# Optimization experiments

Hardware: AMD Instinct MI355X
Metric: run time of the kernel (lower is better)

The kernel has to match this reference:

```python
import jax, jax.numpy as jnp
import numpy as np

IS_CAUSAL = True
NEG_INF = float('-inf')


def setup_inputs() -> dict:
    key = jax.random.key(0)
    kq, kk, kv = jax.random.split(key, 3)
    B, H, S, D = 4, 16, 2048, 64
    return {
        'query': jax.random.normal(kq, (B, H, S, D), dtype=jnp.float32),
        'key': jax.random.normal(kk, (B, H, S, D), dtype=jnp.float32),
        'value': jax.random.normal(kv, (B, H, S, D), dtype=jnp.float32),
    }


def reference(query, key, value):
    # Attention(Q,K,V) = softmax(QK^T / sqrt(d_k) + causal_mask) V
    d_k = query.shape[-1]
    scale = 1.0 / np.sqrt(d_k).astype(np.float32)
    # [B,H,Sq,Sk]
    scores = jnp.einsum('bhqd,bhkd->bhqk', query, key) * scale
    if IS_CAUSAL:
        sq, sk = query.shape[-2], key.shape[-2]
        causal = jnp.triu(jnp.ones((sq, sk), dtype=bool), k=1)
        scores = jnp.where(causal[None, None, :, :], NEG_INF, scores)
    weights = jax.nn.softmax(scores, axis=-1)
    # dropout p=0.0 (eval): identity
    out = jnp.einsum('bhqk,bhkd->bhqd', weights, value)
    return out
```

## Files before the change

### kernel.cpp

```cpp
#include <hip/hip_runtime.h>
#include <stdint.h>


#define SLEN 2048
#define DHEAD 64
#define NHEADS 64
#define NELEM (SLEN * DHEAD * NHEADS)
#define PADP 72

typedef short bf16x8 __attribute__((ext_vector_type(8)));
typedef float f32x4 __attribute__((ext_vector_type(4)));

__device__ __forceinline__ uint32_t pkbf(float hi, float lo) {
    uint32_t a = __builtin_bit_cast(uint32_t, lo) + 0x8000u;
    uint32_t b = __builtin_bit_cast(uint32_t, hi) + 0x8000u;
    return __builtin_amdgcn_perm(b, a, 0x07060302u);
}
__device__ __forceinline__ unsigned short f2bf(float f) {
    return (unsigned short)((__builtin_bit_cast(uint32_t, f) + 0x8000u) >> 16);
}
__device__ __forceinline__ int swz(int row, int g) {
    return row * 64 + ((g ^ (row & 7)) << 3);
}

__global__ __launch_bounds__(256)
void convert_prep(const float* __restrict__ K, const float* __restrict__ V,
                  unsigned short* __restrict__ Kb, unsigned short* __restrict__ Vtb) {
    __shared__ unsigned short Lt[64 * 264];
    const int b = blockIdx.x, t = threadIdx.x;
    if (b < 4096) {
        const int off = (b * 256 + t) * 8;
        float4 a = *(const float4*)(K + off);
        float4 c = *(const float4*)(K + off + 4);
        uint4 o;
        o.x = pkbf(a.y, a.x); o.y = pkbf(a.w, a.z);
        o.z = pkbf(c.y, c.x); o.w = pkbf(c.w, c.z);
        *(uint4*)(Kb + off) = o;
    } else {
        const int vb2 = b - 4096;
        const int head = vb2 >> 3, kblk = vb2 & 7;
        const float* Vh = V + (size_t)head * (SLEN * DHEAD) + kblk * 256 * DHEAD;
        unsigned short* Vo = Vtb + (size_t)head * (SLEN * DHEAD) + kblk * 256;
#pragma unroll
        for (int i = 0; i < 16; ++i) {
            int idx = t + 256 * i;
            int key = idx >> 4, d4 = idx & 15;
            float4 v = *(const float4*)(Vh + key * DHEAD + d4 * 4);
            Lt[(d4 * 4 + 0) * 264 + key] = f2bf(v.x);
            Lt[(d4 * 4 + 1) * 264 + key] = f2bf(v.y);
            Lt[(d4 * 4 + 2) * 264 + key] = f2bf(v.z);
            Lt[(d4 * 4 + 3) * 264 + key] = f2bf(v.w);
        }
        __syncthreads();
#pragma unroll
        for (int jj = 0; jj < 8; ++jj) {
            int idx = t + 256 * jj;
            int d = idx >> 5, k8 = idx & 31;
            *(uint4*)(Vo + (size_t)d * SLEN + k8 * 8) = *(const uint4*)(Lt + d * 264 + k8 * 8);
        }
    }
}

__global__ __launch_bounds__(256, 4)
void sdpa_mfma(const float* __restrict__ Qf, const unsigned short* __restrict__ Kb,
               const unsigned short* __restrict__ Vtb, float* __restrict__ Og) {
    const int n = blockIdx.x;
    const int j = n >> 8, c = n & 255;
    const int head = c & 63;
    const int A  = (c >> 6) + 4 * j;
    const int Bq = 31 - A;

    const size_t hb = (size_t)head * SLEN * DHEAD;
    const float* Qh = Qf + hb;
    const unsigned short* Kh  = Kb + hb;
    const unsigned short* Vth = Vtb + hb;
    float* Oh = Og + hb;

    const int tid  = threadIdx.x;
    const int w    = tid >> 6, lane = tid & 63;
    const int cl   = lane & 15, quad = lane >> 4;

    __shared__ unsigned short Kl[64 * 64];
    __shared__ unsigned short Vt[64 * 64];
    __shared__ unsigned short Pl[4 * 32 * PADP];

    const int qw = ((w < 2) ? A * 64 : Bq * 64) + (w & 1) * 32;
    unsigned short* Plw = Pl + w * 32 * PADP;

    const float SCL = 0.18033688f;

    bf16x8 qf[2][2];
#pragma unroll
    for (int m = 0; m < 2; ++m)
#pragma unroll
        for (int h = 0; h < 2; ++h) {
            const float* src = Qh + (size_t)(qw + m * 16 + cl) * DHEAD + h * 32 + quad * 8;
            float4 a = *(const float4*)src;
            float4 b = *(const float4*)(src + 4);
            uint4 u;
            u.x = pkbf(a.y * SCL, a.x * SCL); u.y = pkbf(a.w * SCL, a.z * SCL);
            u.z = pkbf(b.y * SCL, b.x * SCL); u.w = pkbf(b.w * SCL, b.z * SCL);
            qf[m][h] = __builtin_bit_cast(bf16x8, u);
        }

    f32x4 o[2][4];
#pragma unroll
    for (int m = 0; m < 2; ++m)
#pragma unroll
        for (int d = 0; d < 4; ++d) o[m][d] = (f32x4){0.f, 0.f, 0.f, 0.f};
    float ls[2] = {0.f, 0.f};

    const int p1 = tid + 256;
    const int srow0 = tid >> 3, sg0 = tid & 7;
    const int srow1 = p1 >> 3,  sg1 = p1 & 7;
    const int lo0 = swz(srow0, sg0), lo1 = swz(srow1, sg1);
    const size_t kS0 = (size_t)srow0 * DHEAD + sg0 * 8, kS1 = (size_t)srow1 * DHEAD + sg1 * 8;
    const size_t vS0 = (size_t)srow0 * SLEN + sg0 * 8,  vS1 = (size_t)srow1 * SLEN + sg1 * 8;

    const int ntiles = Bq + 1;
    uint4 kr0 = *(const uint4*)(Kh + kS0), kr1 = *(const uint4*)(Kh + kS1);
    uint4 vr0 = *(const uint4*)(Vth + vS0), vr1 = *(const uint4*)(Vth + vS1);

    for (int t = 0; t < ntiles; ++t) {
        const int k0 = t * 64;
        __syncthreads();
        *(uint4*)(Kl + lo0) = kr0; *(uint4*)(Kl + lo1) = kr1;
        *(uint4*)(Vt + lo0) = vr0; *(uint4*)(Vt + lo1) = vr1;
        __syncthreads();
        if (t + 1 < ntiles) {
            const size_t ko = (size_t)(k0 + 64) * DHEAD;
            kr0 = *(const uint4*)(Kh + kS0 + ko);
            kr1 = *(const uint4*)(Kh + kS1 + ko);
            vr0 = *(const uint4*)(Vth + vS0 + (k0 + 64));
            vr1 = *(const uint4*)(Vth + vS1 + (k0 + 64));
        }
        if (k0 > qw + 31) continue;
        const bool partial = (k0 + 63 > qw);

#pragma unroll
        for (int kk = 0; kk < 4; ++kk) {
            bf16x8 kb0 = __builtin_bit_cast(bf16x8, *(const uint4*)(Kl + swz(kk * 16 + cl, quad)));
            bf16x8 kb1 = __builtin_bit_cast(bf16x8, *(const uint4*)(Kl + swz(kk * 16 + cl, 4 + quad)));
            const int krel = kk * 16 + quad * 4;
#pragma unroll
            for (int qq = 0; qq < 2; ++qq) {
                f32x4 s = (f32x4){0.f, 0.f, 0.f, 0.f};
                s = __builtin_amdgcn_mfma_f32_16x16x32_bf16(kb0, qf[qq][0], s, 0, 0, 0);
                s = __builtin_amdgcn_mfma_f32_16x16x32_bf16(kb1, qf[qq][1], s, 0, 0, 0);
                float p0, p1v, p2, p3;
                if (partial) {
                    const int qrel = qw - k0 + qq * 16 + cl;
                    p0 = (krel + 0 <= qrel) ? __builtin_amdgcn_exp2f(s[0]) : 0.f;
                    p1v = (krel + 1 <= qrel) ? __builtin_amdgcn_exp2f(s[1]) : 0.f;
                    p2 = (krel + 2 <= qrel) ? __builtin_amdgcn_exp2f(s[2]) : 0.f;
                    p3 = (krel + 3 <= qrel) ? __builtin_amdgcn_exp2f(s[3]) : 0.f;
                } else {
                    p0 = __builtin_amdgcn_exp2f(s[0]);
                    p1v = __builtin_amdgcn_exp2f(s[1]);
                    p2 = __builtin_amdgcn_exp2f(s[2]);
                    p3 = __builtin_amdgcn_exp2f(s[3]);
                }
                ls[qq] += (p0 + p1v) + (p2 + p3);
                uint2 pw;
                asm("v_cvt_pk_bf16_f32 %0, %1, %2" : "=v"(pw.x) : "v"(p0), "v"(p1v));
                asm("v_cvt_pk_bf16_f32 %0, %1, %2" : "=v"(pw.y) : "v"(p2), "v"(p3));
                *(uint2*)(Plw + (qq * 16 + cl) * PADP + kk * 16 + quad * 4) = pw;
            }
        }

        bf16x8 pa[2][2];
#pragma unroll
        for (int m = 0; m < 2; ++m)
#pragma unroll
            for (int h = 0; h < 2; ++h)
                pa[m][h] = __builtin_bit_cast(bf16x8,
                    *(const uint4*)(Plw + (m * 16 + cl) * PADP + h * 32 + quad * 8));
#pragma unroll
        for (int dd = 0; dd < 4; ++dd) {
            bf16x8 vb0 = __builtin_bit_cast(bf16x8, *(const uint4*)(Vt + swz(dd * 16 + cl, quad)));
            bf16x8 vb1 = __builtin_bit_cast(bf16x8, *(const uint4*)(Vt + swz(dd * 16 + cl, 4 + quad)));
#pragma unroll
            for (int m = 0; m < 2; ++m) {
                o[m][dd] = __builtin_amdgcn_mfma_f32_16x16x32_bf16(pa[m][0], vb0, o[m][dd], 0, 0, 0);
                o[m][dd] = __builtin_amdgcn_mfma_f32_16x16x32_bf16(pa[m][1], vb1, o[m][dd], 0, 0, 0);
            }
        }
    }

#pragma unroll
    for (int qq = 0; qq < 2; ++qq) {
        float v = ls[qq];
        v += __shfl_xor(v, 16);
        v += __shfl_xor(v, 32);
        ls[qq] = v;
    }

#pragma unroll
    for (int m = 0; m < 2; ++m)
#pragma unroll
        for (int r = 0; r < 4; ++r) {
            const float inv = 1.0f / __shfl(ls[m], quad * 4 + r);
#pragma unroll
            for (int dd = 0; dd < 4; ++dd)
                Oh[(size_t)(qw + m * 16 + quad * 4 + r) * DHEAD + dd * 16 + cl] = o[m][dd][r] * inv;
        }
}

extern "C" void kernel_launch(void* const* d_in, const int* in_sizes, int n_in,
                              void* d_out, int out_size, void* d_ws, size_t ws_size,
                              hipStream_t stream) {
    const float* Q = (const float*)d_in[0];
    const float* K = (const float*)d_in[1];
    const float* V = (const float*)d_in[2];
    float*       O = (float*)d_out;

    unsigned short* Kbf  = (unsigned short*)d_ws;
    unsigned short* Vtbf = Kbf + NELEM;

    convert_prep<<<dim3(4096 + 512), dim3(256), 0, stream>>>(K, V, Kbf, Vtbf);
    sdpa_mfma<<<dim3(1024), dim3(256), 0, stream>>>(Q, Kbf, Vtbf, O);
}
```

Measured before the change: 190.2 us.

## Feed softmax probabilities to PV MFMA directly from registers, dropping LDS round-trip

Result: no change. 193.0 us (+1.5%).

```diff
diff --git a/kernel.cpp b/kernel.cpp
--- a/kernel.cpp
+++ b/kernel.cpp
@@ -6,9 +6,9 @@
 #define DHEAD 64
 #define NHEADS 64
 #define NELEM (SLEN * DHEAD * NHEADS)
-#define PADP 72
 
 typedef short bf16x8 __attribute__((ext_vector_type(8)));
+typedef short bf16x4 __attribute__((ext_vector_type(4)));
 typedef float f32x4 __attribute__((ext_vector_type(4)));
 
 __device__ __forceinline__ uint32_t pkbf(float hi, float lo) {
@@ -21,6 +21,15 @@
 }
 __device__ __forceinline__ int swz(int row, int g) {
     return row * 64 + ((g ^ (row & 7)) << 3);
+}
+
+__device__ __forceinline__ f32x4 mfma16(bf16x4 a, bf16x4 b, f32x4 c) {
+#if __has_builtin(__builtin_amdgcn_mfma_f32_16x16x16bf16_1k)
+    return __builtin_amdgcn_mfma_f32_16x16x16bf16_1k(a, b, c, 0, 0, 0);
+#else
+    asm("v_mfma_f32_16x16x16_bf16 %0, %1, %2, %0" : "+v"(c) : "v"(a), "v"(b));
+    return c;
+#endif
 }
 
 __global__ __launch_bounds__(256)
@@ -82,10 +91,8 @@
 
     __shared__ unsigned short Kl[64 * 64];
     __shared__ unsigned short Vt[64 * 64];
-    __shared__ unsigned short Pl[4 * 32 * PADP];
 
     const int qw = ((w < 2) ? A * 64 : Bq * 64) + (w & 1) * 32;
-    unsigned short* Plw = Pl + w * 32 * PADP;
 
     const float SCL = 0.18033688f;
 
@@ -142,6 +149,7 @@
             bf16x8 kb0 = __builtin_bit_cast(bf16x8, *(const uint4*)(Kl + swz(kk * 16 + cl, quad)));
             bf16x8 kb1 = __builtin_bit_cast(bf16x8, *(const uint4*)(Kl + swz(kk * 16 + cl, 4 + quad)));
             const int krel = kk * 16 + quad * 4;
+            bf16x4 paf[2];
 #pragma unroll
             for (int qq = 0; qq < 2; ++qq) {
                 f32x4 s = (f32x4){0.f, 0.f, 0.f, 0.f};
@@ -164,25 +172,16 @@
                 uint2 pw;
                 asm("v_cvt_pk_bf16_f32 %0, %1, %2" : "=v"(pw.x) : "v"(p0), "v"(p1v));
                 asm("v_cvt_pk_bf16_f32 %0, %1, %2" : "=v"(pw.y) : "v"(p2), "v"(p3));
-                *(uint2*)(Plw + (qq * 16 + cl) * PADP + kk * 16 + quad * 4) = pw;
+                paf[qq] = __builtin_bit_cast(bf16x4, pw);
             }
-        }
-
-        bf16x8 pa[2][2];
-#pragma unroll
-        for (int m = 0; m < 2; ++m)
-#pragma unroll
-            for (int h = 0; h < 2; ++h)
-                pa[m][h] = __builtin_bit_cast(bf16x8,
-                    *(const uint4*)(Plw + (m * 16 + cl) * PADP + h * 32 + quad * 8));
-#pragma unroll
-        for (int dd = 0; dd < 4; ++dd) {
-            bf16x8 vb0 = __builtin_bit_cast(bf16x8, *(const uint4*)(Vt + swz(dd * 16 + cl, quad)));
-            bf16x8 vb1 = __builtin_bit_cast(bf16x8, *(const uint4*)(Vt + swz(dd * 16 + cl, 4 + quad)));
-#pragma unroll
-            for (int m = 0; m < 2; ++m) {
-                o[m][dd] = __builtin_amdgcn_mfma_f32_16x16x32_bf16(pa[m][0], vb0, o[m][dd], 0, 0, 0);
-                o[m][dd] = __builtin_amdgcn_mfma_f32_16x16x32_bf16(pa[m][1], vb1, o[m][dd], 0, 0, 0);
+#pragma unroll
+            for (int dd = 0; dd < 4; ++dd) {
+                const int vrow = dd * 16 + cl;
+                const unsigned short* vp = Vt + vrow * 64
+                    + ((((2 * kk + (quad >> 1)) ^ (cl & 7)) << 3) + (quad & 1) * 4);
+                bf16x4 vb = __builtin_bit_cast(bf16x4, *(const uint2*)vp);
+                o[0][dd] = mfma16(paf[0], vb, o[0][dd]);
+                o[1][dd] = mfma16(paf[1], vb, o[1][dd]);
             }
         }
     }
```

## Process four causal query tiles per 512-thread block to share K/V staging

Applied to the files above, without the earlier changes.

Result: slower. 195.4 us (+2.7%).

```diff
diff --git a/kernel.cpp b/kernel.cpp
--- a/kernel.cpp
+++ b/kernel.cpp
@@ -61,14 +61,12 @@
     }
 }
 
-__global__ __launch_bounds__(256, 4)
+__global__ __launch_bounds__(512, 4)
 void sdpa_mfma(const float* __restrict__ Qf, const unsigned short* __restrict__ Kb,
                const unsigned short* __restrict__ Vtb, float* __restrict__ Og) {
     const int n = blockIdx.x;
-    const int j = n >> 8, c = n & 255;
-    const int head = c & 63;
-    const int A  = (c >> 6) + 4 * j;
-    const int Bq = 31 - A;
+    const int head = n >> 3;
+    const int A    = n & 7;
 
     const size_t hb = (size_t)head * SLEN * DHEAD;
     const float* Qh = Qf + hb;
@@ -82,9 +80,11 @@
 
     __shared__ unsigned short Kl[64 * 64];
     __shared__ unsigned short Vt[64 * 64];
-    __shared__ unsigned short Pl[4 * 32 * PADP];
-
-    const int qw = ((w < 2) ? A * 64 : Bq * 64) + (w & 1) * 32;
+    __shared__ unsigned short Pl[8 * 32 * PADP];
+
+    const int tsel = w >> 1;
+    const int tile = 16 * (tsel >> 1) + ((tsel & 1) ? (15 - A) : A);
+    const int qw   = tile * 64 + (w & 1) * 32;
     unsigned short* Plw = Pl + w * 32 * PADP;
 
     const float SCL = 0.18033688f;
@@ -110,29 +110,25 @@
         for (int d = 0; d < 4; ++d) o[m][d] = (f32x4){0.f, 0.f, 0.f, 0.f};
     float ls[2] = {0.f, 0.f};
 
-    const int p1 = tid + 256;
     const int srow0 = tid >> 3, sg0 = tid & 7;
-    const int srow1 = p1 >> 3,  sg1 = p1 & 7;
-    const int lo0 = swz(srow0, sg0), lo1 = swz(srow1, sg1);
-    const size_t kS0 = (size_t)srow0 * DHEAD + sg0 * 8, kS1 = (size_t)srow1 * DHEAD + sg1 * 8;
-    const size_t vS0 = (size_t)srow0 * SLEN + sg0 * 8,  vS1 = (size_t)srow1 * SLEN + sg1 * 8;
-
-    const int ntiles = Bq + 1;
-    uint4 kr0 = *(const uint4*)(Kh + kS0), kr1 = *(const uint4*)(Kh + kS1);
-    uint4 vr0 = *(const uint4*)(Vth + vS0), vr1 = *(const uint4*)(Vth + vS1);
+    const int lo0 = swz(srow0, sg0);
+    const size_t kS0 = (size_t)srow0 * DHEAD + sg0 * 8;
+    const size_t vS0 = (size_t)srow0 * SLEN + sg0 * 8;
+
+    const int ntiles = 32 - A;
+    uint4 kr0 = *(const uint4*)(Kh + kS0);
+    uint4 vr0 = *(const uint4*)(Vth + vS0);
 
     for (int t = 0; t < ntiles; ++t) {
         const int k0 = t * 64;
         __syncthreads();
-        *(uint4*)(Kl + lo0) = kr0; *(uint4*)(Kl + lo1) = kr1;
-        *(uint4*)(Vt + lo0) = vr0; *(uint4*)(Vt + lo1) = vr1;
+        *(uint4*)(Kl + lo0) = kr0;
+        *(uint4*)(Vt + lo0) = vr0;
         __syncthreads();
         if (t + 1 < ntiles) {
             const size_t ko = (size_t)(k0 + 64) * DHEAD;
             kr0 = *(const uint4*)(Kh + kS0 + ko);
-            kr1 = *(const uint4*)(Kh + kS1 + ko);
             vr0 = *(const uint4*)(Vth + vS0 + (k0 + 64));
-            vr1 = *(const uint4*)(Vth + vS1 + (k0 + 64));
         }
         if (k0 > qw + 31) continue;
         const bool partial = (k0 + 63 > qw);
@@ -218,5 +214,5 @@
     unsigned short* Vtbf = Kbf + NELEM;
 
     convert_prep<<<dim3(4096 + 512), dim3(256), 0, stream>>>(K, V, Kbf, Vtbf);
-    sdpa_mfma<<<dim3(1024), dim3(256), 0, stream>>>(Q, Kbf, Vtbf, O);
-}
+    sdpa_mfma<<<dim3(512), dim3(512), 0, stream>>>(Q, Kbf, Vtbf, O);
+}
```
